# Performance work log

Hardware: AMD Instinct MI355X
Metric: run time of the kernel (lower is better)

Reference implementation:

```python
import jax, jax.numpy as jnp
import numpy as np
import math

EMBED_DIM = 512
NHEAD = 8
HEAD_DIM = EMBED_DIM // NHEAD
B, L = 32, 512
EPS = 1e-5


def layer_norm(x, gamma, beta):
    mu = jnp.mean(x, axis=-1, keepdims=True)
    var = jnp.var(x, axis=-1, keepdims=True)
    return (x - mu) * jax.lax.rsqrt(var + EPS) * gamma + beta


def setup_inputs() -> dict:
    key = jax.random.key(0)
    ks = jax.random.split(key, 16)
    D = EMBED_DIM
    s = 1.0 / math.sqrt(D)
    return {
        "x": jax.random.normal(ks[0], (B, L, D), dtype=jnp.float32),
        "inter": jax.random.normal(ks[1], (B, L, L, 4), dtype=jnp.float32),
        "qkv_w": jax.random.normal(ks[2], (D, 3 * D), dtype=jnp.float32) * s,
        "qkv_b": jnp.zeros((3 * D,), dtype=jnp.float32),
        "out_w": jax.random.normal(ks[3], (D, D), dtype=jnp.float32) * s,
        "out_b": jnp.zeros((D,), dtype=jnp.float32),
        "norm1_g": jnp.ones((D,), dtype=jnp.float32),
        "norm1_b": jnp.zeros((D,), dtype=jnp.float32),
        "norm2_g": jnp.ones((D,), dtype=jnp.float32),
        "norm2_b": jnp.zeros((D,), dtype=jnp.float32),
        "inter_w": jax.random.normal(ks[4], (4, NHEAD), dtype=jnp.float32) * 0.5,
        "ffn_w1": jax.random.normal(ks[5], (D, 4 * D), dtype=jnp.float32) * s,
        "ffn_b1": jnp.zeros((4 * D,), dtype=jnp.float32),
        "ffn_w2": jax.random.normal(ks[6], (4 * D, D), dtype=jnp.float32) * (1.0 / math.sqrt(4 * D)),
        "ffn_b2": jnp.zeros((D,), dtype=jnp.float32),
    }


def reference(x, inter, qkv_w, qkv_b, out_w, out_b, norm1_g, norm1_b,
              norm2_g, norm2_b, inter_w, ffn_w1, ffn_b1, ffn_w2, ffn_b2):
    Bb, Ll, D = x.shape
    residual = x
    h = layer_norm(x, norm1_g, norm1_b)
    qkv = (h @ qkv_w + qkv_b).reshape(Bb, Ll, 3, NHEAD, HEAD_DIM)
    qkv = jnp.transpose(qkv, (2, 0, 3, 1, 4))  # (3, B, H, L, hd)
    q, k, v = qkv[0], qkv[1], qkv[2]
    scale = math.sqrt(HEAD_DIM)
    scores = jnp.einsum("bhqd,bhkd->bhqk", q, k) / scale
    # pairwise interaction bias: (B,L,L,4) @ (4,H) -> (B,H,L,L)
    bias = jnp.einsum("bqkf,fh->bhqk", inter, inter_w)
    attn = jax.nn.softmax(scores + bias, axis=-1)
    # dropout p=0 in eval mode
    out = jnp.einsum("bhqk,bhkd->bhqd", attn, v)
    out = jnp.transpose(out, (0, 2, 1, 3)).reshape(Bb, Ll, D)
    x = residual + out @ out_w + out_b
    h2 = layer_norm(x, norm2_g, norm2_b)
    ffn = jax.nn.gelu(h2 @ ffn_w1 + ffn_b1, approximate=False) @ ffn_w2 + ffn_b2
    return x + ffn
```

## Files before the change

### kernel.cpp

```cpp
#include <hip/hip_runtime.h>
#include <math.h>

#define BB 32
#define LL 512
#define DD 512
#define NH 8
#define HD 64

typedef __attribute__((ext_vector_type(8))) short bf16x8;
typedef __attribute__((ext_vector_type(4))) float f32x4;

__device__ __forceinline__ unsigned short f2bf(float x) {
    union { float f; unsigned u; } v; v.f = x;
    unsigned r = v.u + 0x7fffu + ((v.u >> 16) & 1u);
    return (unsigned short)(r >> 16);
}

__device__ __forceinline__ float warp_sum(float v) {
    #pragma unroll
    for (int o = 32; o > 0; o >>= 1) v += __shfl_down(v, o);
    return v;
}

__global__ void ln_kernel(const float* __restrict__ X, const float* __restrict__ g,
                          const float* __restrict__ b, unsigned short* __restrict__ Y) {
    __shared__ float red[8];
    const size_t base = (size_t)blockIdx.x * DD;
    const int t = threadIdx.x;
    float x0 = X[base + t], x1 = X[base + t + 256];
    float s = warp_sum(x0 + x1);
    float q = warp_sum(x0 * x0 + x1 * x1);
    if ((t & 63) == 0) { red[t >> 6] = s; red[4 + (t >> 6)] = q; }
    __syncthreads();
    float S = red[0] + red[1] + red[2] + red[3];
    float Q = red[4] + red[5] + red[6] + red[7];
    float mu  = S * (1.0f / 512.0f);
    float var = Q * (1.0f / 512.0f) - mu * mu;
    float r = rsqrtf(var + 1e-5f);
    Y[base + t]       = f2bf((x0 - mu) * r * g[t] + b[t]);
    Y[base + t + 256] = f2bf((x1 - mu) * r * g[t + 256] + b[t + 256]);
}

__global__ void transpose_bf16(const float* __restrict__ W, unsigned short* __restrict__ WT,
                               int K, int N) {
    __shared__ float t[32][33];
    const int n0 = blockIdx.x * 32, k0 = blockIdx.y * 32;
    const int tx = threadIdx.x & 31, ty = threadIdx.x >> 5;
    #pragma unroll
    for (int r = 0; r < 32; r += 8)
        t[ty + r][tx] = W[(size_t)(k0 + ty + r) * N + n0 + tx];
    __syncthreads();
    #pragma unroll
    for (int r = 0; r < 32; r += 8)
        WT[(size_t)(n0 + ty + r) * K + k0 + tx] = f2bf(t[tx][ty + r]);
}

template <int ACT, int RES, int OM>
__global__ __launch_bounds__(256)
void gemm_mfma(const unsigned short* __restrict__ A, const unsigned short* __restrict__ BT,
               const float* __restrict__ bias, const float* __restrict__ res,
               void* __restrict__ Cv, unsigned short* __restrict__ kfrag,
               unsigned short* __restrict__ vfrag, int M, int N, int K) {
    __shared__ unsigned short As[128 * 64];
    __shared__ unsigned short Bs[128 * 64];
    const int tid = threadIdx.x;
    const int wave = tid >> 6, lane = tid & 63;
    const int wm = (wave >> 1) * 64, wn = (wave & 1) * 64;
    const int bm = blockIdx.y * 128, bn = blockIdx.x * 128;

    f32x4 acc[4][4] = {};

    for (int k0 = 0; k0 < K; k0 += 64) {
        __syncthreads();
        #pragma unroll
        for (int it = 0; it < 4; ++it) {
            const int s = it * 256 + tid;
            const int row = s >> 3, pch = s & 7;
            const int lch = pch ^ (row & 7);
            const unsigned short* ga = A + (size_t)(bm + row) * K + k0 + lch * 8;
            __builtin_amdgcn_global_load_lds(
                (const __attribute__((address_space(1))) void*)ga,
                (__attribute__((address_space(3))) void*)(As + s * 8), 16, 0, 0);
            const unsigned short* gb = BT + (size_t)(bn + row) * K + k0 + lch * 8;
            __builtin_amdgcn_global_load_lds(
                (const __attribute__((address_space(1))) void*)gb,
                (__attribute__((address_space(3))) void*)(Bs + s * 8), 16, 0, 0);
        }
        __syncthreads();
        #pragma unroll
        for (int ks = 0; ks < 2; ++ks) {
            bf16x8 af[4], bfr[4];
            #pragma unroll
            for (int i = 0; i < 4; ++i) {
                const int row = wm + i * 16 + (lane & 15);
                const int pch = (ks * 4 + (lane >> 4)) ^ (row & 7);
                af[i] = *(const bf16x8*)(As + row * 64 + pch * 8);
            }
            #pragma unroll
            for (int j = 0; j < 4; ++j) {
                const int row = wn + j * 16 + (lane & 15);
                const int pch = (ks * 4 + (lane >> 4)) ^ (row & 7);
                bfr[j] = *(const bf16x8*)(Bs + row * 64 + pch * 8);
            }
            #pragma unroll
            for (int i = 0; i < 4; ++i)
                #pragma unroll
                for (int j = 0; j < 4; ++j)
                    acc[i][j] = __builtin_amdgcn_mfma_f32_16x16x32_bf16(
                        af[i], bfr[j], acc[i][j], 0, 0, 0);
        }
    }

    const int cl = lane & 15, rq = (lane >> 4) * 4;
    #pragma unroll
    for (int j = 0; j < 4; ++j) {
        const int col = bn + wn + j * 16 + cl;
        const float bv = bias[col];
        #pragma unroll
        for (int i = 0; i < 4; ++i) {
            const int r0 = bm + wm + i * 16 + rq;
            #pragma unroll
            for (int r = 0; r < 4; ++r) {
                float v = acc[i][j][r] + bv;
                if (ACT == 1) v = 0.5f * v * (1.0f + erff(v * 0.70710678118654752f));
                if (RES) v += res[(size_t)(r0 + r) * N + col];
                if (OM == 0) {
                    ((float*)Cv)[(size_t)(r0 + r) * N + col] = v;
                } else if (OM == 1) {
                    ((unsigned short*)Cv)[(size_t)(r0 + r) * N + col] = f2bf(v);
                } else {
                    const int row = r0 + r;
                    const int b = row >> 9, kpos = row & 511;
                    if (col < 512) {
                        ((unsigned short*)Cv)[(size_t)row * 512 + col] = f2bf(v);
                    } else if (col < 1024) {
                        const int h = (col - 512) >> 6, dd = (col - 512) & 63;
                        const int kt = kpos >> 6, jj = (kpos >> 4) & 3, lo2 = kpos & 15;
                        const int kk = dd >> 5, hi2 = (dd >> 3) & 3, e = dd & 7;
                        kfrag[((((size_t)(b * NH + h) * 8 + kt) * 2 + kk) * 4 + jj) * 512
                              + (hi2 * 16 + lo2) * 8 + e] = f2bf(v);
                    } else {
                        const int h = (col - 1024) >> 6, dd = (col - 1024) & 63;
                        const int kt = kpos >> 6, kk = (kpos >> 5) & 1, hi2 = (kpos >> 3) & 3, e = kpos & 7;
                        const int jj = dd >> 4, lo2 = dd & 15;
                        vfrag[((((size_t)(b * NH + h) * 8 + kt) * 2 + kk) * 4 + jj) * 512
                              + (hi2 * 16 + lo2) * 8 + e] = f2bf(v);
                    }
                }
            }
        }
    }
}

__global__ __launch_bounds__(512)
void flash_kernel(const unsigned short* __restrict__ qbuf,
                  const unsigned short* __restrict__ kfrag,
                  const unsigned short* __restrict__ vfrag,
                  const float* __restrict__ inter,
                  const float* __restrict__ iw,
                  unsigned short* __restrict__ O) {
    __shared__ float itile[2][16 * 256];
    __shared__ unsigned short plds[8][16 * 72];
    const int qg = blockIdx.x, b = blockIdx.y;
    const int tid = threadIdx.x, wave = tid >> 6, lane = tid & 63;
    const int h = wave;
    const int lo = lane & 15, hi = lane >> 4;
    const int qA  = qg * 16 + lo;
    const int qC0 = qg * 16 + hi * 4;

    const float iw0 = iw[h], iw1 = iw[8 + h], iw2 = iw[16 + h], iw3 = iw[24 + h];

    const float* interb = inter + (size_t)b * 512 * 512 * 4;
    unsigned short* pw = &plds[wave][0];

    const unsigned short* qp = qbuf + ((size_t)(b * 512 + qA)) * 512 + h * 64 + hi * 8;
    const bf16x8 qf0 = *(const bf16x8*)(qp);
    const bf16x8 qf1 = *(const bf16x8*)(qp + 32);

    f32x4 o[4] = {};
    float m[4] = {-1e30f, -1e30f, -1e30f, -1e30f};
    float lsum[4] = {};

    #pragma unroll
    for (int i = 0; i < 2; ++i) {
        const int row = wave * 2 + i;
        const float* src = interb + ((size_t)(qg * 16 + row) * 512 + 0) * 4 + lane * 4;
        __builtin_amdgcn_global_load_lds(
            (const __attribute__((address_space(1))) void*)src,
            (__attribute__((address_space(3))) void*)(&itile[0][row * 256] + lane * 4),
            16, 0, 0);
    }

    for (int kt = 0; kt < 8; ++kt) {
        const int kb = kt * 64;
        const int buf = kt & 1;
        const size_t fb = (((size_t)(b * NH + h) * 8 + kt) * 2) * 4 * 512;
        __syncthreads();
        if (kt < 7) {
            #pragma unroll
            for (int i = 0; i < 2; ++i) {
                const int row = wave * 2 + i;
                const float* src = interb + ((size_t)(qg * 16 + row) * 512 + kb + 64) * 4 + lane * 4;
                __builtin_amdgcn_global_load_lds(
                    (const __attribute__((address_space(1))) void*)src,
                    (__attribute__((address_space(3))) void*)(&itile[buf ^ 1][row * 256] + lane * 4),
                    16, 0, 0);
            }
        }
        f32x4 s[4] = {};
        #pragma unroll
        for (int kk = 0; kk < 2; ++kk) {
            const bf16x8 qf = kk ? qf1 : qf0;
            #pragma unroll
            for (int j = 0; j < 4; ++j) {
                bf16x8 kf = *(const bf16x8*)(kfrag + fb + (size_t)(kk * 4 + j) * 512 + lane * 8);
                s[j] = __builtin_amdgcn_mfma_f32_16x16x32_bf16(qf, kf, s[j], 0, 0, 0);
            }
        }
        float sv[4][4];
        #pragma unroll
        for (int j = 0; j < 4; ++j) {
            #pragma unroll
            for (int r = 0; r < 4; ++r) {
                const float4 f = *(const float4*)&itile[buf][(hi * 4 + r) * 256 + (j * 16 + lo) * 4];
                sv[j][r] = s[j][r] * 0.125f + f.x * iw0 + f.y * iw1 + f.z * iw2 + f.w * iw3;
            }
        }
        float alpha[4];
        #pragma unroll
        for (int r = 0; r < 4; ++r) {
            float t = fmaxf(fmaxf(sv[0][r], sv[1][r]), fmaxf(sv[2][r], sv[3][r]));
            #pragma unroll
            for (int off = 1; off < 16; off <<= 1) t = fmaxf(t, __shfl_xor(t, off));
            const float mn = fmaxf(m[r], t);
            alpha[r] = __expf(m[r] - mn);
            m[r] = mn;
        }
        float p[4][4];
        #pragma unroll
        for (int j = 0; j < 4; ++j)
            #pragma unroll
            for (int r = 0; r < 4; ++r)
                p[j][r] = __expf(sv[j][r] - m[r]);
        #pragma unroll
        for (int r = 0; r < 4; ++r) {
            float t = p[0][r] + p[1][r] + p[2][r] + p[3][r];
            #pragma unroll
            for (int off = 1; off < 16; off <<= 1) t += __shfl_xor(t, off);
            lsum[r] = lsum[r] * alpha[r] + t;
        }
        #pragma unroll
        for (int j2 = 0; j2 < 4; ++j2) {
            o[j2][0] *= alpha[0]; o[j2][1] *= alpha[1];
            o[j2][2] *= alpha[2]; o[j2][3] *= alpha[3];
        }
        #pragma unroll
        for (int j = 0; j < 4; ++j)
            #pragma unroll
            for (int r = 0; r < 4; ++r)
                pw[(hi * 4 + r) * 72 + j * 16 + lo] = f2bf(p[j][r]);
        #pragma unroll
        for (int kk = 0; kk < 2; ++kk) {
            const bf16x8 pf = *(const bf16x8*)(pw + lo * 72 + kk * 32 + hi * 8);
            #pragma unroll
            for (int j2 = 0; j2 < 4; ++j2) {
                bf16x8 vf = *(const bf16x8*)(vfrag + fb + (size_t)(kk * 4 + j2) * 512 + lane * 8);
                o[j2] = __builtin_amdgcn_mfma_f32_16x16x32_bf16(pf, vf, o[j2], 0, 0, 0);
            }
        }
    }
    float inv[4];
    #pragma unroll
    for (int r = 0; r < 4; ++r) inv[r] = 1.0f / lsum[r];
    #pragma unroll
    for (int j2 = 0; j2 < 4; ++j2)
        #pragma unroll
        for (int r = 0; r < 4; ++r)
            O[(size_t)(b * 512 + qC0 + r) * 512 + h * 64 + j2 * 16 + lo] = f2bf(o[j2][r] * inv[r]);
}

extern "C" void kernel_launch(void* const* d_in, const int* in_sizes, int n_in,
                              void* d_out, int out_size, void* d_ws, size_t ws_size,
                              hipStream_t stream) {
    const float* x     = (const float*)d_in[0];
    const float* inter = (const float*)d_in[1];
    const float* qkv_w = (const float*)d_in[2];
    const float* qkv_b = (const float*)d_in[3];
    const float* out_w = (const float*)d_in[4];
    const float* out_b = (const float*)d_in[5];
    const float* n1g   = (const float*)d_in[6];
    const float* n1b   = (const float*)d_in[7];
    const float* n2g   = (const float*)d_in[8];
    const float* n2b   = (const float*)d_in[9];
    const float* iw    = (const float*)d_in[10];
    const float* fw1   = (const float*)d_in[11];
    const float* fb1   = (const float*)d_in[12];
    const float* fw2   = (const float*)d_in[13];
    const float* fb2   = (const float*)d_in[14];
    float* out = (float*)d_out;

    if (ws_size < 190840832ull) return;
    char* ws = (char*)d_ws;
    unsigned short* qbuf    = (unsigned short*)(ws);
    unsigned short* kfrag   = (unsigned short*)(ws + 16777216ull);
    unsigned short* vfrag   = (unsigned short*)(ws + 33554432ull);
    unsigned short* attnout = (unsigned short*)(ws + 50331648ull);
    float*          x2      = (float*)(ws + 67108864ull);
    unsigned short* h_bf    = (unsigned short*)(ws + 100663296ull);
    unsigned short* ffnmid  = (unsigned short*)(ws + 117440512ull);
    unsigned short* qkv_wT  = (unsigned short*)(ws + 184549376ull);
    unsigned short* out_wT  = (unsigned short*)(ws + 186122240ull);
    unsigned short* fw1T    = (unsigned short*)(ws + 186646528ull);
    unsigned short* fw2T    = (unsigned short*)(ws + 188743680ull);

    const int M = BB * LL;

    transpose_bf16<<<dim3(1536 / 32, 512 / 32), 256, 0, stream>>>(qkv_w, qkv_wT, 512, 1536);
    transpose_bf16<<<dim3(512 / 32, 512 / 32), 256, 0, stream>>>(out_w, out_wT, 512, 512);
    transpose_bf16<<<dim3(2048 / 32, 512 / 32), 256, 0, stream>>>(fw1, fw1T, 512, 2048);
    transpose_bf16<<<dim3(512 / 32, 2048 / 32), 256, 0, stream>>>(fw2, fw2T, 2048, 512);
    ln_kernel<<<M, 256, 0, stream>>>(x, n1g, n1b, h_bf);
    gemm_mfma<0, 0, 2><<<dim3(1536 / 128, M / 128), 256, 0, stream>>>(
        h_bf, qkv_wT, qkv_b, nullptr, qbuf, kfrag, vfrag, M, 1536, 512);
    flash_kernel<<<dim3(LL / 16, BB), 512, 0, stream>>>(qbuf, kfrag, vfrag, inter, iw, attnout);
    gemm_mfma<0, 1, 0><<<dim3(512 / 128, M / 128), 256, 0, stream>>>(
        attnout, out_wT, out_b, x, x2, nullptr, nullptr, M, 512, 512);
    ln_kernel<<<M, 256, 0, stream>>>(x2, n2g, n2b, h_bf);
    gemm_mfma<1, 0, 1><<<dim3(2048 / 128, M / 128), 256, 0, stream>>>(
        h_bf, fw1T, fb1, nullptr, ffnmid, nullptr, nullptr, M, 2048, 512);
    gemm_mfma<0, 1, 0><<<dim3(512 / 128, M / 128), 256, 0, stream>>>(
        ffnmid, fw2T, fb2, x2, out, nullptr, nullptr, M, 512, 2048);
}
```

Baseline: 572.2 us.

## Transpose score MFMA, register-prefetch bias tiles, and hoist K/V fragment loads

Swaps the MFMA operand order so each lane holds a full query row of scores. Row max and sum then need only two cross-lane shuffles instead of four per row, and packed bf16 stores write P. K and V fragments are loaded up front into registers with sched barriers and raised wave priority around the MFMAs. The interaction-bias tile prefetch moves from global_load_lds into registers with a padded LDS layout (stride 260) to cut bank conflicts. The cost is higher register pressure and manual scheduling constraints that could reduce occupancy or overlap.

Result: faster. 546.6 us (-4.5%).

```diff
diff --git a/kernel.cpp b/kernel.cpp
--- a/kernel.cpp
+++ b/kernel.cpp
@@ -159,124 +159,150 @@
                   const float* __restrict__ inter,
                   const float* __restrict__ iw,
                   unsigned short* __restrict__ O) {
-    __shared__ float itile[2][16 * 256];
+    __shared__ float it0[16 * 260];
+    __shared__ float it1[16 * 260];
     __shared__ unsigned short plds[8][16 * 72];
     const int qg = blockIdx.x, b = blockIdx.y;
     const int tid = threadIdx.x, wave = tid >> 6, lane = tid & 63;
     const int h = wave;
     const int lo = lane & 15, hi = lane >> 4;
-    const int qA  = qg * 16 + lo;
-    const int qC0 = qg * 16 + hi * 4;
 
     const float iw0 = iw[h], iw1 = iw[8 + h], iw2 = iw[16 + h], iw3 = iw[24 + h];
-
     const float* interb = inter + (size_t)b * 512 * 512 * 4;
     unsigned short* pw = &plds[wave][0];
 
-    const unsigned short* qp = qbuf + ((size_t)(b * 512 + qA)) * 512 + h * 64 + hi * 8;
+    const unsigned short* qp = qbuf + ((size_t)(b * 512 + qg * 16 + lo)) * 512 + h * 64 + hi * 8;
     const bf16x8 qf0 = *(const bf16x8*)(qp);
     const bf16x8 qf1 = *(const bf16x8*)(qp + 32);
 
+    const int srow = wave * 2;
+    const float* src0 = interb + ((size_t)(qg * 16 + srow) * 512) * 4 + lane * 4;
+    const float* src1 = interb + ((size_t)(qg * 16 + srow + 1) * 512) * 4 + lane * 4;
+
     f32x4 o[4] = {};
-    float m[4] = {-1e30f, -1e30f, -1e30f, -1e30f};
-    float lsum[4] = {};
-
-    #pragma unroll
-    for (int i = 0; i < 2; ++i) {
-        const int row = wave * 2 + i;
-        const float* src = interb + ((size_t)(qg * 16 + row) * 512 + 0) * 4 + lane * 4;
-        __builtin_amdgcn_global_load_lds(
-            (const __attribute__((address_space(1))) void*)src,
-            (__attribute__((address_space(3))) void*)(&itile[0][row * 256] + lane * 4),
-            16, 0, 0);
-    }
-
-    for (int kt = 0; kt < 8; ++kt) {
-        const int kb = kt * 64;
-        const int buf = kt & 1;
-        const size_t fb = (((size_t)(b * NH + h) * 8 + kt) * 2) * 4 * 512;
+    float m = -1e30f, lsum = 0.0f;
+
+    {
+        const float4 a0 = *(const float4*)src0;
+        const float4 a1 = *(const float4*)src1;
+        *(float4*)(it0 + srow * 260 + lane * 4) = a0;
+        *(float4*)(it0 + (srow + 1) * 260 + lane * 4) = a1;
+    }
+
+    auto iter = [&](int kt, const float* __restrict__ rd, float* __restrict__ st) {
+        const size_t fb = (((size_t)((b * NH + h) * 8 + kt)) * 2) * 4 * 512;
         __syncthreads();
+        bf16x8 kf0[4], kf1[4];
+        #pragma unroll
+        for (int j = 0; j < 4; ++j)
+            kf0[j] = *(const bf16x8*)(kfrag + fb + (size_t)j * 512 + lane * 8);
+        #pragma unroll
+        for (int j = 0; j < 4; ++j)
+            kf1[j] = *(const bf16x8*)(kfrag + fb + (size_t)(4 + j) * 512 + lane * 8);
+        __builtin_amdgcn_sched_barrier(0);
+        f32x4 s[4] = {};
+        __builtin_amdgcn_s_setprio(1);
+        #pragma unroll
+        for (int j = 0; j < 4; ++j)
+            s[j] = __builtin_amdgcn_mfma_f32_16x16x32_bf16(kf0[j], qf0, s[j], 0, 0, 0);
+        #pragma unroll
+        for (int j = 0; j < 4; ++j)
+            s[j] = __builtin_amdgcn_mfma_f32_16x16x32_bf16(kf1[j], qf1, s[j], 0, 0, 0);
+        __builtin_amdgcn_s_setprio(0);
+        const float4* brow = (const float4*)(rd + lo * 260);
+        #pragma unroll
+        for (int j = 0; j < 4; ++j)
+            #pragma unroll
+            for (int r = 0; r < 4; ++r) {
+                const float4 f = brow[j * 16 + hi * 4 + r];
+                s[j][r] = s[j][r] * 0.125f + f.x * iw0 + f.y * iw1 + f.z * iw2 + f.w * iw3;
+            }
+        bf16x8 vf0[4], vf1[4];
+        #pragma unroll
+        for (int j = 0; j < 4; ++j)
+            vf0[j] = *(const bf16x8*)(vfrag + fb + (size_t)j * 512 + lane * 8);
+        #pragma unroll
+        for (int j = 0; j < 4; ++j)
+            vf1[j] = *(const bf16x8*)(vfrag + fb + (size_t)(4 + j) * 512 + lane * 8);
+        __builtin_amdgcn_sched_barrier(0);
+        float4 sn0, sn1;
         if (kt < 7) {
-            #pragma unroll
-            for (int i = 0; i < 2; ++i) {
-                const int row = wave * 2 + i;
-                const float* src = interb + ((size_t)(qg * 16 + row) * 512 + kb + 64) * 4 + lane * 4;
-                __builtin_amdgcn_global_load_lds(
-                    (const __attribute__((address_space(1))) void*)src,
-                    (__attribute__((address_space(3))) void*)(&itile[buf ^ 1][row * 256] + lane * 4),
-                    16, 0, 0);
-            }
-        }
-        f32x4 s[4] = {};
-        #pragma unroll
-        for (int kk = 0; kk < 2; ++kk) {
-            const bf16x8 qf = kk ? qf1 : qf0;
-            #pragma unroll
-            for (int j = 0; j < 4; ++j) {
-                bf16x8 kf = *(const bf16x8*)(kfrag + fb + (size_t)(kk * 4 + j) * 512 + lane * 8);
-                s[j] = __builtin_amdgcn_mfma_f32_16x16x32_bf16(qf, kf, s[j], 0, 0, 0);
-            }
-        }
-        float sv[4][4];
+            sn0 = *(const float4*)(src0 + (kt + 1) * 256);
+            sn1 = *(const float4*)(src1 + (kt + 1) * 256);
+        }
+        __builtin_amdgcn_sched_barrier(0);
+        float t0 = fmaxf(fmaxf(s[0][0], s[0][1]), fmaxf(s[0][2], s[0][3]));
+        float t1 = fmaxf(fmaxf(s[1][0], s[1][1]), fmaxf(s[1][2], s[1][3]));
+        float t2 = fmaxf(fmaxf(s[2][0], s[2][1]), fmaxf(s[2][2], s[2][3]));
+        float t3 = fmaxf(fmaxf(s[3][0], s[3][1]), fmaxf(s[3][2], s[3][3]));
+        float mx = fmaxf(fmaxf(t0, t1), fmaxf(t2, t3));
+        mx = fmaxf(mx, __shfl_xor(mx, 16));
+        mx = fmaxf(mx, __shfl_xor(mx, 32));
+        const float mn = fmaxf(m, mx);
+        const float al = __expf(m - mn);
+        m = mn;
+        #pragma unroll
+        for (int j = 0; j < 4; ++j)
+            #pragma unroll
+            for (int r = 0; r < 4; ++r)
+                s[j][r] = __expf(s[j][r] - mn);
+        float u0 = (s[0][0] + s[0][1]) + (s[0][2] + s[0][3]);
+        float u1 = (s[1][0] + s[1][1]) + (s[1][2] + s[1][3]);
+        float u2 = (s[2][0] + s[2][1]) + (s[2][2] + s[2][3]);
+        float u3 = (s[3][0] + s[3][1]) + (s[3][2] + s[3][3]);
+        float ts = (u0 + u1) + (u2 + u3);
+        ts += __shfl_xor(ts, 16);
+        ts += __shfl_xor(ts, 32);
+        lsum = lsum * al + ts;
+        const float aR0 = __shfl(al, hi * 4 + 0);
+        const float aR1 = __shfl(al, hi * 4 + 1);
+        const float aR2 = __shfl(al, hi * 4 + 2);
+        const float aR3 = __shfl(al, hi * 4 + 3);
+        #pragma unroll
+        for (int j2 = 0; j2 < 4; ++j2) {
+            o[j2][0] *= aR0; o[j2][1] *= aR1; o[j2][2] *= aR2; o[j2][3] *= aR3;
+        }
+        uint2* pq = (uint2*)(pw + lo * 72);
         #pragma unroll
         for (int j = 0; j < 4; ++j) {
-            #pragma unroll
-            for (int r = 0; r < 4; ++r) {
-                const float4 f = *(const float4*)&itile[buf][(hi * 4 + r) * 256 + (j * 16 + lo) * 4];
-                sv[j][r] = s[j][r] * 0.125f + f.x * iw0 + f.y * iw1 + f.z * iw2 + f.w * iw3;
-            }
-        }
-        float alpha[4];
-        #pragma unroll
-        for (int r = 0; r < 4; ++r) {
-            float t = fmaxf(fmaxf(sv[0][r], sv[1][r]), fmaxf(sv[2][r], sv[3][r]));
-            #pragma unroll
-            for (int off = 1; off < 16; off <<= 1) t = fmaxf(t, __shfl_xor(t, off));
-            const float mn = fmaxf(m[r], t);
-            alpha[r] = __expf(m[r] - mn);
-            m[r] = mn;
-        }
-        float p[4][4];
-        #pragma unroll
-        for (int j = 0; j < 4; ++j)
-            #pragma unroll
-            for (int r = 0; r < 4; ++r)
-                p[j][r] = __expf(sv[j][r] - m[r]);
-        #pragma unroll
-        for (int r = 0; r < 4; ++r) {
-            float t = p[0][r] + p[1][r] + p[2][r] + p[3][r];
-            #pragma unroll
-            for (int off = 1; off < 16; off <<= 1) t += __shfl_xor(t, off);
-            lsum[r] = lsum[r] * alpha[r] + t;
-        }
-        #pragma unroll
-        for (int j2 = 0; j2 < 4; ++j2) {
-            o[j2][0] *= alpha[0]; o[j2][1] *= alpha[1];
-            o[j2][2] *= alpha[2]; o[j2][3] *= alpha[3];
-        }
-        #pragma unroll
-        for (int j = 0; j < 4; ++j)
-            #pragma unroll
-            for (int r = 0; r < 4; ++r)
-                pw[(hi * 4 + r) * 72 + j * 16 + lo] = f2bf(p[j][r]);
+            uint2 d;
+            d.x = (unsigned)f2bf(s[j][0]) | ((unsigned)f2bf(s[j][1]) << 16);
+            d.y = (unsigned)f2bf(s[j][2]) | ((unsigned)f2bf(s[j][3]) << 16);
+            pq[j * 4 + hi] = d;
+        }
+        __builtin_amdgcn_s_setprio(1);
         #pragma unroll
         for (int kk = 0; kk < 2; ++kk) {
             const bf16x8 pf = *(const bf16x8*)(pw + lo * 72 + kk * 32 + hi * 8);
             #pragma unroll
-            for (int j2 = 0; j2 < 4; ++j2) {
-                bf16x8 vf = *(const bf16x8*)(vfrag + fb + (size_t)(kk * 4 + j2) * 512 + lane * 8);
-                o[j2] = __builtin_amdgcn_mfma_f32_16x16x32_bf16(pf, vf, o[j2], 0, 0, 0);
-            }
-        }
-    }
-    float inv[4];
-    #pragma unroll
-    for (int r = 0; r < 4; ++r) inv[r] = 1.0f / lsum[r];
-    #pragma unroll
-    for (int j2 = 0; j2 < 4; ++j2)
-        #pragma unroll
-        for (int r = 0; r < 4; ++r)
-            O[(size_t)(b * 512 + qC0 + r) * 512 + h * 64 + j2 * 16 + lo] = f2bf(o[j2][r] * inv[r]);
+            for (int j2 = 0; j2 < 4; ++j2)
+                o[j2] = __builtin_amdgcn_mfma_f32_16x16x32_bf16(
+                    pf, kk ? vf1[j2] : vf0[j2], o[j2], 0, 0, 0);
+        }
+        __builtin_amdgcn_s_setprio(0);
+        if (kt < 7) {
+            *(float4*)(st + srow * 260 + lane * 4) = sn0;
+            *(float4*)(st + (srow + 1) * 260 + lane * 4) = sn1;
+        }
+    };
+
+    for (int kt2 = 0; kt2 < 4; ++kt2) {
+        iter(kt2 * 2, it0, it1);
+        iter(kt2 * 2 + 1, it1, it0);
+    }
+
+    const float iR0 = 1.0f / __shfl(lsum, hi * 4 + 0);
+    const float iR1 = 1.0f / __shfl(lsum, hi * 4 + 1);
+    const float iR2 = 1.0f / __shfl(lsum, hi * 4 + 2);
+    const float iR3 = 1.0f / __shfl(lsum, hi * 4 + 3);
+    const int qC0 = qg * 16 + hi * 4;
+    #pragma unroll
+    for (int j2 = 0; j2 < 4; ++j2) {
+        O[(size_t)(b * 512 + qC0 + 0) * 512 + h * 64 + j2 * 16 + lo] = f2bf(o[j2][0] * iR0);
+        O[(size_t)(b * 512 + qC0 + 1) * 512 + h * 64 + j2 * 16 + lo] = f2bf(o[j2][1] * iR1);
+        O[(size_t)(b * 512 + qC0 + 2) * 512 + h * 64 + j2 * 16 + lo] = f2bf(o[j2][2] * iR2);
+        O[(size_t)(b * 512 + qC0 + 3) * 512 + h * 64 + j2 * 16 + lo] = f2bf(o[j2][3] * iR3);
+    }
 }
 
 extern "C" void kernel_launch(void* const* d_in, const int* in_sizes, int n_in,
```
